# Kernel tuning notes

Hardware: AMD Instinct MI355X
Metric: run time of the kernel (lower is better)

Reference implementation:

```python
import jax, jax.numpy as jnp
import numpy as np

NEG = -1000000000.0

def setup_inputs() -> dict:
    key = jax.random.key(0)
    k1, k2, k3, k4, k5, k6 = jax.random.split(key, 6)
    B, T, H = 32, 4096, 512
    scale = 1.0 / np.sqrt(H)
    return {
        "enc_seq": jax.random.normal(k1, (B, T, H), dtype=jnp.float32),
        "enc_mask": jax.random.randint(k2, (B, T), 0, 2, dtype=jnp.int32),
        "dec_state": jax.random.normal(k3, (B, H), dtype=jnp.float32),
        "W_h": jax.random.normal(k4, (H, H), dtype=jnp.float32) * scale,
        "W_s": jax.random.normal(k5, (H, H), dtype=jnp.float32) * scale,
        "v": jax.random.normal(k6, (H,), dtype=jnp.float32) * scale,
    }

def reference(enc_seq, enc_mask, dec_state, W_h, W_s, v):
    # torch nn.Linear computes x @ W.T; weights here stored as (out, in) = (H, H)
    h = jnp.einsum("bth,oh->bto", enc_seq, W_h)          # [B,T,H]
    s = jnp.einsum("bh,oh->bo", dec_state, W_s)[:, None]  # [B,1,H]
    e = jnp.einsum("bth,h->bt", jnp.tanh(h + s), v)       # [B,T]
    e = jnp.where(enc_mask == 0, NEG, e)
    a = jax.nn.softmax(e, axis=1)                          # [B,T]
    ctx = jnp.einsum("bt,bth->bh", a, enc_seq)             # [B,H]
    return ctx
```

## Files before the change

kernel.cpp:

```cpp
#include <hip/hip_runtime.h>
#include <hip/hip_bf16.h>

#define B_ 32
#define T_ 4096
#define H_ 512
#define NEGV (-1000000000.0f)

using bf16x8  = __attribute__((ext_vector_type(8))) __bf16;
using short8  = __attribute__((ext_vector_type(8))) short;
using f32x4   = __attribute__((ext_vector_type(4))) float;

static __device__ __forceinline__ short f2bf(float f) {
    unsigned u = __builtin_bit_cast(unsigned, f);
    unsigned r = (u + 0x7fffu + ((u >> 16) & 1u)) >> 16;
    return (short)r;
}

static __device__ __forceinline__ float tanh_fast(float x) {
    float e = __builtin_amdgcn_exp2f(x * 2.8853900817779268f);
    return 1.0f - 2.0f * __builtin_amdgcn_rcpf(e + 1.0f);
}

static __device__ __forceinline__ f32x4 mfma16(short8 a, short8 b, f32x4 c) {
    return __builtin_amdgcn_mfma_f32_16x16x32_bf16(
        __builtin_bit_cast(bf16x8, a), __builtin_bit_cast(bf16x8, b), c, 0, 0, 0);
}

#define GLOAD_LDS16(g, l)                                                     \
    __builtin_amdgcn_global_load_lds(                                         \
        (const __attribute__((address_space(1))) unsigned*)(g),               \
        (__attribute__((address_space(3))) unsigned*)(l), 16, 0, 0)

__global__ __launch_bounds__(256) void wh_prep(const float* __restrict__ Wh,
                                               short* __restrict__ Whp) {
    int id = blockIdx.x * 256 + threadIdx.x;
    int n = id >> 6, kc = id & 63;
    const float4* src = (const float4*)(Wh + (size_t)n * H_ + kc * 8);
    float4 f0 = src[0];
    float4 f1 = src[1];
    short8 t;
    t[0] = f2bf(f0.x); t[1] = f2bf(f0.y); t[2] = f2bf(f0.z); t[3] = f2bf(f0.w);
    t[4] = f2bf(f1.x); t[5] = f2bf(f1.y); t[6] = f2bf(f1.z); t[7] = f2bf(f1.w);
    int nc = n >> 5, r = n & 31;
    *(short8*)(Whp + nc * 16384 + r * 512 + ((kc ^ (n & 7)) << 3)) = t;
}

__global__ __launch_bounds__(256) void s_kernel(const float* __restrict__ dec,
                                                const float* __restrict__ Ws,
                                                float* __restrict__ s_out) {
    __shared__ float dec_l[H_];
    int b = blockIdx.y;
    int tid = threadIdx.x;
    dec_l[tid]       = dec[b * H_ + tid];
    dec_l[tid + 256] = dec[b * H_ + tid + 256];
    __syncthreads();
    int o = blockIdx.x * 256 + tid;
    const float4* w = (const float4*)(Ws + (size_t)o * H_);
    float acc = 0.f;
#pragma unroll 8
    for (int k = 0; k < H_ / 4; ++k) {
        float4 wv = w[k];
        acc += wv.x * dec_l[4 * k] + wv.y * dec_l[4 * k + 1] +
               wv.z * dec_l[4 * k + 2] + wv.w * dec_l[4 * k + 3];
    }
    s_out[b * H_ + o] = acc;
}

__global__ __launch_bounds__(256, 2) void e_kernel(const float* __restrict__ enc,
                                                   const int* __restrict__ mask,
                                                   const short* __restrict__ Whp,
                                                   const float* __restrict__ s_in,
                                                   const float* __restrict__ v,
                                                   float* __restrict__ e_out) {
    __shared__ short lds_b[2][32 * 512];
    __shared__ float s_l[H_];
    __shared__ float v_l[H_];

    const int tid  = threadIdx.x;
    const int wave = tid >> 6;
    const int lane = tid & 63;
    const int q    = lane >> 4;
    const int lq   = lane & 15;
    const int key  = lq & 7;

    const int row0 = blockIdx.x * 128;
    const int b    = row0 / T_;

    for (int i = tid; i < H_; i += 256) {
        s_l[i] = s_in[b * H_ + i];
        v_l[i] = v[i];
    }

    short8 afrag[2][16];
#pragma unroll
    for (int g = 0; g < 2; ++g) {
        int m = row0 + wave * 32 + g * 16 + lq;
        const float* ap = enc + (size_t)m * H_ + q * 8;
#pragma unroll
        for (int ks = 0; ks < 16; ++ks) {
            float4 f0 = *(const float4*)(ap + ks * 32);
            float4 f1 = *(const float4*)(ap + ks * 32 + 4);
            short8 t;
            t[0] = f2bf(f0.x); t[1] = f2bf(f0.y); t[2] = f2bf(f0.z); t[3] = f2bf(f0.w);
            t[4] = f2bf(f1.x); t[5] = f2bf(f1.y); t[6] = f2bf(f1.z); t[7] = f2bf(f1.w);
            afrag[g][ks] = t;
        }
    }

    {
        const char* gsrc = (const char*)Whp;
#pragma unroll
        for (int j = 0; j < 8; ++j) {
            int off = wave * 8192 + j * 1024;
            GLOAD_LDS16(gsrc + off + lane * 16, (char*)lds_b[0] + off);
        }
    }

    float e_acc[2][4] = {};
    __syncthreads();

    for (int nt = 0; nt < 16; ++nt) {
        if (nt < 15) {
            const char* gsrc = (const char*)Whp + (nt + 1) * 32768;
            short* dst = lds_b[(nt + 1) & 1];
#pragma unroll
            for (int j = 0; j < 8; ++j) {
                int off = wave * 8192 + j * 1024;
                GLOAD_LDS16(gsrc + off + lane * 16, (char*)dst + off);
            }
        }
        const short* cur = lds_b[nt & 1];
#pragma unroll
        for (int s = 0; s < 2; ++s) {
            const short* rowp = cur + (s * 16 + lq) * 512;
            f32x4 acc0 = {0.f, 0.f, 0.f, 0.f};
            f32x4 acc1 = {0.f, 0.f, 0.f, 0.f};
#pragma unroll
            for (int ks = 0; ks < 16; ++ks) {
                short8 bf = *(const short8*)(rowp + (((ks * 4 + q) ^ key) << 3));
                acc0 = mfma16(afrag[0][ks], bf, acc0);
                acc1 = mfma16(afrag[1][ks], bf, acc1);
            }
            int n = nt * 32 + s * 16 + lq;
            float sv = s_l[n];
            float vv = v_l[n];
#pragma unroll
            for (int r = 0; r < 4; ++r) {
                e_acc[0][r] += tanh_fast(acc0[r] + sv) * vv;
                e_acc[1][r] += tanh_fast(acc1[r] + sv) * vv;
            }
        }
        __syncthreads();
    }

#pragma unroll
    for (int g = 0; g < 2; ++g)
#pragma unroll
        for (int r = 0; r < 4; ++r) {
            float t = e_acc[g][r];
            t += __shfl_xor(t, 1, 16);
            t += __shfl_xor(t, 2, 16);
            t += __shfl_xor(t, 4, 16);
            t += __shfl_xor(t, 8, 16);
            if (lq == 0) {
                int m = row0 + wave * 32 + g * 16 + q * 4 + r;
                e_out[m] = mask[m] ? t : NEGV;
            }
        }
}

__global__ __launch_bounds__(256) void softmax_kernel(float* __restrict__ e) {
    __shared__ float red[256];
    int b = blockIdx.x, tid = threadIdx.x;
    float* eb = e + (size_t)b * T_;
    float m = -3.4e38f;
    for (int i = tid; i < T_; i += 256) m = fmaxf(m, eb[i]);
    red[tid] = m;
    __syncthreads();
    for (int s = 128; s > 0; s >>= 1) {
        if (tid < s) red[tid] = fmaxf(red[tid], red[tid + s]);
        __syncthreads();
    }
    m = red[0];
    __syncthreads();
    float sum = 0.f;
    for (int i = tid; i < T_; i += 256) {
        float p = __builtin_amdgcn_exp2f((eb[i] - m) * 1.4426950408889634f);
        eb[i] = p;
        sum += p;
    }
    red[tid] = sum;
    __syncthreads();
    for (int s = 128; s > 0; s >>= 1) {
        if (tid < s) red[tid] += red[tid + s];
        __syncthreads();
    }
    float inv = 1.0f / red[0];
    for (int i = tid; i < T_; i += 256) eb[i] *= inv;
}

__global__ __launch_bounds__(256) void ctx_kernel(const float* __restrict__ enc,
                                                  const float* __restrict__ a,
                                                  float* __restrict__ out) {
    constexpr int TC = 128;
    __shared__ float a_l[TC];
    int b = blockIdx.y, tc = blockIdx.x;
    int tid = threadIdx.x;
    int t0 = tc * TC;
    if (tid < TC) a_l[tid] = a[(size_t)b * T_ + t0 + tid];
    __syncthreads();
    const float2* ep = (const float2*)(enc + ((size_t)b * T_ + t0) * H_) + tid;
    float2 acc = {0.f, 0.f};
#pragma unroll 8
    for (int t = 0; t < TC; ++t) {
        float2 v2 = ep[(size_t)t * (H_ / 2)];
        float w = a_l[t];
        acc.x += w * v2.x;
        acc.y += w * v2.y;
    }
    atomicAdd(&out[b * H_ + 2 * tid], acc.x);
    atomicAdd(&out[b * H_ + 2 * tid + 1], acc.y);
}

extern "C" void kernel_launch(void* const* d_in, const int* in_sizes, int n_in,
                              void* d_out, int out_size, void* d_ws, size_t ws_size,
                              hipStream_t stream) {
    (void)in_sizes; (void)n_in; (void)ws_size;
    const float* enc  = (const float*)d_in[0];
    const int*   mask = (const int*)d_in[1];
    const float* dec  = (const float*)d_in[2];
    const float* Wh   = (const float*)d_in[3];
    const float* Ws   = (const float*)d_in[4];
    const float* v    = (const float*)d_in[5];
    float* out = (float*)d_out;

    short* whp_buf = (short*)d_ws;
    float* s_buf   = (float*)(whp_buf + 512 * 512);
    float* e_buf   = s_buf + B_ * H_;

    wh_prep<<<dim3(128), 256, 0, stream>>>(Wh, whp_buf);
    s_kernel<<<dim3(2, B_), 256, 0, stream>>>(dec, Ws, s_buf);
    e_kernel<<<dim3(B_ * T_ / 128), 256, 0, stream>>>(enc, mask, whp_buf, s_buf, v, e_buf);
    softmax_kernel<<<dim3(B_), 256, 0, stream>>>(e_buf);
    hipMemsetAsync(d_out, 0, (size_t)out_size * sizeof(float), stream);
    ctx_kernel<<<dim3(T_ / 128, B_), 256, 0, stream>>>(enc, e_buf, out);
}
```

Measured before the change: 507.1 us.

## Fuse softmax and context into score kernel with online-softmax partials and combine

Each 128-row score block now does a local max/sum softmax in shared memory and immediately computes a partial context from the enc rows it already covers. It writes per-block partial contexts plus max/sum stats, and a small combine kernel rescales and reduces them per batch. This removes the separate softmax and context kernels, the memset and the atomics, and it rereads the block's enc tile while it is likely still in cache. Separately, the W_h bf16 prep now writes data pre-arranged in MFMA fragment order, so B-operand LDS reads become linear per lane instead of XOR-swizzled row reads, at the possible cost of LDS bank conflicts.

```diff
diff --git a/kernel.cpp b/kernel.cpp
--- a/kernel.cpp
+++ b/kernel.cpp
@@ -5,6 +5,7 @@
 #define T_ 4096
 #define H_ 512
 #define NEGV (-1000000000.0f)
+#define LOG2E 1.4426950408889634f
 
 using bf16x8  = __attribute__((ext_vector_type(8))) __bf16;
 using short8  = __attribute__((ext_vector_type(8))) short;
@@ -34,15 +35,19 @@
 __global__ __launch_bounds__(256) void wh_prep(const float* __restrict__ Wh,
                                                short* __restrict__ Whp) {
     int id = blockIdx.x * 256 + threadIdx.x;
-    int n = id >> 6, kc = id & 63;
-    const float4* src = (const float4*)(Wh + (size_t)n * H_ + kc * 8);
+    int nc  = id >> 11;
+    int rem = id & 2047;
+    int f   = rem >> 6;
+    int l   = rem & 63;
+    int n  = nc * 32 + (f >> 4) * 16 + (l & 15);
+    int k0 = (f & 15) * 32 + (l >> 4) * 8;
+    const float4* src = (const float4*)(Wh + (size_t)n * H_ + k0);
     float4 f0 = src[0];
     float4 f1 = src[1];
     short8 t;
     t[0] = f2bf(f0.x); t[1] = f2bf(f0.y); t[2] = f2bf(f0.z); t[3] = f2bf(f0.w);
     t[4] = f2bf(f1.x); t[5] = f2bf(f1.y); t[6] = f2bf(f1.z); t[7] = f2bf(f1.w);
-    int nc = n >> 5, r = n & 31;
-    *(short8*)(Whp + nc * 16384 + r * 512 + ((kc ^ (n & 7)) << 3)) = t;
+    *(short8*)(Whp + (size_t)id * 8) = t;
 }
 
 __global__ __launch_bounds__(256) void s_kernel(const float* __restrict__ dec,
@@ -66,25 +71,26 @@
     s_out[b * H_ + o] = acc;
 }
 
-__global__ __launch_bounds__(256, 2) void e_kernel(const float* __restrict__ enc,
-                                                   const int* __restrict__ mask,
-                                                   const short* __restrict__ Whp,
-                                                   const float* __restrict__ s_in,
-                                                   const float* __restrict__ v,
-                                                   float* __restrict__ e_out) {
+__global__ __launch_bounds__(256, 2) void e_fused(const float* __restrict__ enc,
+                                                  const int* __restrict__ mask,
+                                                  const short* __restrict__ Whp,
+                                                  const float* __restrict__ s_in,
+                                                  const float* __restrict__ v,
+                                                  float* __restrict__ pctx,
+                                                  float* __restrict__ ml) {
     __shared__ short lds_b[2][32 * 512];
     __shared__ float s_l[H_];
     __shared__ float v_l[H_];
+    __shared__ float e_l[128];
 
     const int tid  = threadIdx.x;
     const int wave = tid >> 6;
     const int lane = tid & 63;
     const int q    = lane >> 4;
     const int lq   = lane & 15;
-    const int key  = lq & 7;
 
     const int row0 = blockIdx.x * 128;
-    const int b    = row0 / T_;
+    const int b    = row0 >> 12;
 
     for (int i = tid; i < H_; i += 256) {
         s_l[i] = s_in[b * H_ + i];
@@ -132,12 +138,12 @@
         const short* cur = lds_b[nt & 1];
 #pragma unroll
         for (int s = 0; s < 2; ++s) {
-            const short* rowp = cur + (s * 16 + lq) * 512;
+            const short* fp = cur + s * 8192 + lane * 8;
             f32x4 acc0 = {0.f, 0.f, 0.f, 0.f};
             f32x4 acc1 = {0.f, 0.f, 0.f, 0.f};
 #pragma unroll
             for (int ks = 0; ks < 16; ++ks) {
-                short8 bf = *(const short8*)(rowp + (((ks * 4 + q) ^ key) << 3));
+                short8 bf = *(const short8*)(fp + ks * 512);
                 acc0 = mfma16(afrag[0][ks], bf, acc0);
                 acc1 = mfma16(afrag[1][ks], bf, acc1);
             }
@@ -163,69 +169,76 @@
             t += __shfl_xor(t, 4, 16);
             t += __shfl_xor(t, 8, 16);
             if (lq == 0) {
-                int m = row0 + wave * 32 + g * 16 + q * 4 + r;
-                e_out[m] = mask[m] ? t : NEGV;
-            }
-        }
-}
-
-__global__ __launch_bounds__(256) void softmax_kernel(float* __restrict__ e) {
-    __shared__ float red[256];
-    int b = blockIdx.x, tid = threadIdx.x;
-    float* eb = e + (size_t)b * T_;
-    float m = -3.4e38f;
-    for (int i = tid; i < T_; i += 256) m = fmaxf(m, eb[i]);
-    red[tid] = m;
-    __syncthreads();
-    for (int s = 128; s > 0; s >>= 1) {
-        if (tid < s) red[tid] = fmaxf(red[tid], red[tid + s]);
-        __syncthreads();
-    }
-    m = red[0];
-    __syncthreads();
-    float sum = 0.f;
-    for (int i = tid; i < T_; i += 256) {
-        float p = __builtin_amdgcn_exp2f((eb[i] - m) * 1.4426950408889634f);
-        eb[i] = p;
-        sum += p;
-    }
-    red[tid] = sum;
-    __syncthreads();
-    for (int s = 128; s > 0; s >>= 1) {
-        if (tid < s) red[tid] += red[tid + s];
-        __syncthreads();
-    }
-    float inv = 1.0f / red[0];
-    for (int i = tid; i < T_; i += 256) eb[i] *= inv;
-}
-
-__global__ __launch_bounds__(256) void ctx_kernel(const float* __restrict__ enc,
-                                                  const float* __restrict__ a,
-                                                  float* __restrict__ out) {
-    constexpr int TC = 128;
-    __shared__ float a_l[TC];
-    int b = blockIdx.y, tc = blockIdx.x;
-    int tid = threadIdx.x;
-    int t0 = tc * TC;
-    if (tid < TC) a_l[tid] = a[(size_t)b * T_ + t0 + tid];
-    __syncthreads();
-    const float2* ep = (const float2*)(enc + ((size_t)b * T_ + t0) * H_) + tid;
+                int mr = wave * 32 + g * 16 + q * 4 + r;
+                e_l[mr] = mask[row0 + mr] ? t : NEGV;
+            }
+        }
+    __syncthreads();
+
+    if (wave == 0) {
+        float x0 = e_l[lane];
+        float x1 = e_l[lane + 64];
+        float m = fmaxf(x0, x1);
+#pragma unroll
+        for (int off = 32; off > 0; off >>= 1)
+            m = fmaxf(m, __shfl_xor(m, off, 64));
+        float p0 = __builtin_amdgcn_exp2f((x0 - m) * LOG2E);
+        float p1 = __builtin_amdgcn_exp2f((x1 - m) * LOG2E);
+        float sm = p0 + p1;
+#pragma unroll
+        for (int off = 32; off > 0; off >>= 1)
+            sm += __shfl_xor(sm, off, 64);
+        e_l[lane]      = p0;
+        e_l[lane + 64] = p1;
+        if (lane == 0) {
+            ml[blockIdx.x * 2]     = m;
+            ml[blockIdx.x * 2 + 1] = sm;
+        }
+    }
+    __syncthreads();
+
+    const float2* ep = (const float2*)(enc + (size_t)row0 * H_) + tid;
     float2 acc = {0.f, 0.f};
 #pragma unroll 8
-    for (int t = 0; t < TC; ++t) {
-        float2 v2 = ep[(size_t)t * (H_ / 2)];
-        float w = a_l[t];
+    for (int t = 0; t < 128; ++t) {
+        float w = e_l[t];
+        float2 v2 = ep[(size_t)t * 256];
         acc.x += w * v2.x;
         acc.y += w * v2.y;
     }
-    atomicAdd(&out[b * H_ + 2 * tid], acc.x);
-    atomicAdd(&out[b * H_ + 2 * tid + 1], acc.y);
+    ((float2*)(pctx + (size_t)blockIdx.x * 512))[tid] = acc;
+}
+
+__global__ __launch_bounds__(256) void combine_kernel(const float* __restrict__ pctx,
+                                                      const float* __restrict__ ml,
+                                                      float* __restrict__ out) {
+    int b = blockIdx.x, tid = threadIdx.x;
+    const float* mlb = ml + b * 64;
+    float M = -3.4e38f;
+#pragma unroll
+    for (int j = 0; j < 32; ++j) M = fmaxf(M, mlb[2 * j]);
+    const float2* pc = (const float2*)(pctx + (size_t)b * 32 * 512) + tid;
+    float denom = 0.f;
+    float2 acc = {0.f, 0.f};
+#pragma unroll
+    for (int j = 0; j < 32; ++j) {
+        float w = __builtin_amdgcn_exp2f((mlb[2 * j] - M) * LOG2E);
+        denom += w * mlb[2 * j + 1];
+        float2 p2 = pc[j * 256];
+        acc.x += w * p2.x;
+        acc.y += w * p2.y;
+    }
+    float inv = 1.0f / denom;
+    float2 o;
+    o.x = acc.x * inv;
+    o.y = acc.y * inv;
+    ((float2*)(out + b * H_))[tid] = o;
 }
 
 extern "C" void kernel_launch(void* const* d_in, const int* in_sizes, int n_in,
                               void* d_out, int out_size, void* d_ws, size_t ws_size,
                               hipStream_t stream) {
-    (void)in_sizes; (void)n_in; (void)ws_size;
+    (void)in_sizes; (void)n_in; (void)ws_size; (void)out_size;
     const float* enc  = (const float*)d_in[0];
     const int*   mask = (const int*)d_in[1];
     const float* dec  = (const float*)d_in[2];
@@ -236,12 +249,12 @@
 
     short* whp_buf = (short*)d_ws;
     float* s_buf   = (float*)(whp_buf + 512 * 512);
-    float* e_buf   = s_buf + B_ * H_;
+    float* pctx    = s_buf + B_ * H_;
+    float* ml      = pctx + 1024 * 512;
 
     wh_prep<<<dim3(128), 256, 0, stream>>>(Wh, whp_buf);
     s_kernel<<<dim3(2, B_), 256, 0, stream>>>(dec, Ws, s_buf);
-    e_kernel<<<dim3(B_ * T_ / 128), 256, 0, stream>>>(enc, mask, whp_buf, s_buf, v, e_buf);
-    softmax_kernel<<<dim3(B_), 256, 0, stream>>>(e_buf);
-    hipMemsetAsync(d_out, 0, (size_t)out_size * sizeof(float), stream);
-    ctx_kernel<<<dim3(T_ / 128, B_), 256, 0, stream>>>(enc, e_buf, out);
-}
+    e_fused<<<dim3(B_ * T_ / 128), 256, 0, stream>>>(enc, mask, whp_buf, s_buf, v,
+                                                     pctx, ml);
+    combine_kernel<<<dim3(B_), 256, 0, stream>>>(pctx, ml, out);
+}
```

Result: faster. 485.6 us (-4.2%).
